# Optimization experiments

Measured on AMD Instinct MI355X. Metric: run time of the kernel, lower is better.

## Reference

```python
import jax, jax.numpy as jnp
import numpy as np

NUM_CLASSES = 1000
FEAT_DIM = 128
BATCH = 2048
ALPHA = 1.0


def setup_inputs() -> dict:
    key = jax.random.key(0)
    k1, k2, k3 = jax.random.split(key, 3)
    feat = jax.random.normal(k1, (BATCH, FEAT_DIM), dtype=jnp.float32)
    label = jax.random.randint(k2, (BATCH,), 0, NUM_CLASSES, dtype=jnp.int64)
    # centers ~ kaiming_uniform_(a=sqrt(5)) on a (C, D) matrix -> U(-b, b), b = sqrt(6/((1+5)*D)) = 1/sqrt(D)
    bound = 1.0 / np.sqrt(FEAT_DIM)
    centers = jax.random.uniform(k3, (NUM_CLASSES, FEAT_DIM), dtype=jnp.float32,
                                 minval=-bound, maxval=bound)
    return {"feat": feat, "label": label, "centers": centers}


def reference(feat, label, centers):
    # feat: [B, D], centers: [C, D], label: [B]
    batch_size = feat.shape[0]
    # squared euclidean distance to every center: [B, C]
    diff = feat[:, None, :] - centers[None, :, :]          # [B, C, D]
    dist = jnp.sum(diff * diff, axis=-1)                   # [B, C]
    # margin scaling: multiply true-class distance by (1 + alpha)
    y_onehot = jax.nn.one_hot(label, centers.shape[0], dtype=dist.dtype) * ALPHA + 1.0
    margin_dist = dist * y_onehot
    margin_logits = -0.5 * margin_dist
    logits = -0.5 * dist
    # likelihood regularizer: mean of half squared distance to own center
    cdiff = feat - centers[label]                          # [B, D]
    likelihood = (1.0 / batch_size) * jnp.sum(cdiff * cdiff) / 2.0
    return logits, margin_logits, likelihood
```

## Files before the change

kernel.cpp:

```cpp
#include <hip/hip_runtime.h>

#define BATCH 2048
#define NCLS  1000
#define FEAT  128

typedef short bf16x8 __attribute__((ext_vector_type(8)));
typedef float f32x16 __attribute__((ext_vector_type(16)));

__device__ __forceinline__ unsigned int f2bf(float f) {
    unsigned int u;
    __builtin_memcpy(&u, &f, 4);
    return (u + 0x7fffu + ((u >> 16) & 1u)) >> 16;
}

__device__ __forceinline__ bf16x8 cvt_chunk(const float* __restrict__ p, float& nrm) {
    float4 lo = *(const float4*)p;
    float4 hi = *(const float4*)(p + 4);
    nrm += lo.x * lo.x + lo.y * lo.y + lo.z * lo.z + lo.w * lo.w +
           hi.x * hi.x + hi.y * hi.y + hi.z * hi.z + hi.w * hi.w;
    bf16x8 r;
    r[0] = (short)f2bf(lo.x); r[1] = (short)f2bf(lo.y);
    r[2] = (short)f2bf(lo.z); r[3] = (short)f2bf(lo.w);
    r[4] = (short)f2bf(hi.x); r[5] = (short)f2bf(hi.y);
    r[6] = (short)f2bf(hi.z); r[7] = (short)f2bf(hi.w);
    return r;
}

__global__ __launch_bounds__(256) void lgm_fused(
    const float* __restrict__ feat,
    const float* __restrict__ centers,
    const int* __restrict__ label,
    float* __restrict__ ws,
    float* __restrict__ out)
{
    __shared__ float fn_lds[64];
    __shared__ float red[4];

    int tid     = threadIdx.x;
    int lane    = tid & 63;
    int wave    = tid >> 6;
    int tileCol = blockIdx.x & 15;
    int tileRow = blockIdx.x >> 4;
    int rowBase = tileRow * 64 + (wave & 1) * 32;
    int colBase = tileCol * 64 + (wave >> 1) * 32;
    int m       = lane & 31;
    int half    = lane >> 5;

    int r  = rowBase + m;
    int c0 = colBase + m;
    int c  = (c0 < NCLS) ? c0 : (NCLS - 1);

    const float* ap = feat    + r * FEAT + half * 8;
    const float* bp = centers + c * FEAT + half * 8;

    float fs = 0.0f, cs = 0.0f;
    f32x16 acc = {};
    #pragma unroll
    for (int kk = 0; kk < 8; kk++) {
        bf16x8 a = cvt_chunk(ap + kk * 16, fs);
        bf16x8 b = cvt_chunk(bp + kk * 16, cs);
        acc = __builtin_amdgcn_mfma_f32_32x32x16_bf16(a, b, acc, 0, 0, 0);
    }

    fs += __shfl_xor(fs, 32, 64);
    cs += __shfl_xor(cs, 32, 64);
    fn_lds[(wave & 1) * 32 + m] = fs;
    __syncthreads();

    float* out0 = out;
    float* out1 = out + BATCH * NCLS;
    float cnv   = cs;
    bool  colOK = (c0 < NCLS);
    int   rlb   = (wave & 1) * 32;
    float lsum  = 0.0f;
    #pragma unroll
    for (int reg = 0; reg < 16; reg++) {
        int rl  = rlb + (reg & 3) + 8 * (reg >> 2) + 4 * half;
        int row = tileRow * 64 + rl;
        if (colOK) {
            float dist  = fn_lds[rl] + cnv - 2.0f * acc[reg];
            float logit = -0.5f * dist;
            int   idx   = row * NCLS + c0;
            bool  match = (c0 == label[row]);
            out0[idx] = logit;
            out1[idx] = match ? 2.0f * logit : logit;
            if (match) lsum += dist;
        }
    }

    #pragma unroll
    for (int off = 32; off > 0; off >>= 1) lsum += __shfl_down(lsum, off, 64);
    if (lane == 0) red[wave] = lsum;
    __syncthreads();
    if (tid == 0) ws[blockIdx.x] = red[0] + red[1] + red[2] + red[3];
}

__global__ __launch_bounds__(64) void lgm_finish(
    const float* __restrict__ ws,
    float* __restrict__ out)
{
    int lane = threadIdx.x;
    float s = 0.0f;
    #pragma unroll
    for (int j = 0; j < 8; j++) s += ws[lane + 64 * j];
    #pragma unroll
    for (int off = 32; off > 0; off >>= 1) s += __shfl_down(s, off, 64);
    if (lane == 0) out[2 * BATCH * NCLS] = s * (0.5f / (float)BATCH);
}

extern "C" void kernel_launch(void* const* d_in, const int* in_sizes, int n_in,
                              void* d_out, int out_size, void* d_ws, size_t ws_size,
                              hipStream_t stream) {
    const float* feat    = (const float*)d_in[0];
    const int*   label   = (const int*)d_in[1];
    const float* centers = (const float*)d_in[2];
    float* ws = (float*)d_ws;

    lgm_fused<<<512, 256, 0, stream>>>(feat, centers, label, ws, (float*)d_out);
    lgm_finish<<<1, 64, 0, stream>>>(ws, (float*)d_out);
}
```

Baseline: 75.88 us.

## Stage bf16 tiles in swizzled LDS and compute likelihood directly per row

Each block now loads its 64-row feat tile and 64-row centers tile once with cooperative coalesced loads. It converts them to bf16 and writes them into XOR-swizzled shared memory, then feeds the MFMAs from LDS instead of having each wave reload and reconvert global data. Row and center norms are computed during staging. The likelihood term is now computed exactly in fp32 from feat minus the gathered center, only in tileCol 0 blocks, so the finish kernel reduces 32 partials instead of 512. The cost is about 33KB of LDS per block and an extra barrier, which may reduce occupancy. The kernel is dominated by output stores, so the gain is likely small.

Measured after the change: 71.65 us. 1.06x faster.

```diff
diff --git a/kernel.cpp b/kernel.cpp
--- a/kernel.cpp
+++ b/kernel.cpp
@@ -7,92 +7,149 @@
 typedef short bf16x8 __attribute__((ext_vector_type(8)));
 typedef float f32x16 __attribute__((ext_vector_type(16)));
 
-__device__ __forceinline__ unsigned int f2bf(float f) {
+#define WS_LP 0
+
+__device__ inline unsigned int f2bf(float f) {
     unsigned int u;
     __builtin_memcpy(&u, &f, 4);
     return (u + 0x7fffu + ((u >> 16) & 1u)) >> 16;
 }
 
-__device__ __forceinline__ bf16x8 cvt_chunk(const float* __restrict__ p, float& nrm) {
-    float4 lo = *(const float4*)p;
-    float4 hi = *(const float4*)(p + 4);
-    nrm += lo.x * lo.x + lo.y * lo.y + lo.z * lo.z + lo.w * lo.w +
-           hi.x * hi.x + hi.y * hi.y + hi.z * hi.z + hi.w * hi.w;
-    bf16x8 r;
-    r[0] = (short)f2bf(lo.x); r[1] = (short)f2bf(lo.y);
-    r[2] = (short)f2bf(lo.z); r[3] = (short)f2bf(lo.w);
-    r[4] = (short)f2bf(hi.x); r[5] = (short)f2bf(hi.y);
-    r[6] = (short)f2bf(hi.z); r[7] = (short)f2bf(hi.w);
-    return r;
-}
-
-__global__ __launch_bounds__(256) void lgm_fused(
+__global__ __launch_bounds__(256) void lgm_main_kernel(
     const float* __restrict__ feat,
     const float* __restrict__ centers,
     const int* __restrict__ label,
     float* __restrict__ ws,
     float* __restrict__ out)
 {
-    __shared__ float fn_lds[64];
-    __shared__ float red[4];
+    __shared__ __align__(16) unsigned char smem[33296];
+    unsigned char* sA  = smem;
+    unsigned char* sB  = smem + 16384;
+    float*         sFn = (float*)(smem + 32768);
+    float*         sCn = (float*)(smem + 33024);
+    float*         red = (float*)(smem + 33280);
 
     int tid     = threadIdx.x;
     int lane    = tid & 63;
     int wave    = tid >> 6;
     int tileCol = blockIdx.x & 15;
     int tileRow = blockIdx.x >> 4;
-    int rowBase = tileRow * 64 + (wave & 1) * 32;
-    int colBase = tileCol * 64 + (wave >> 1) * 32;
-    int m       = lane & 31;
-    int half    = lane >> 5;
+    int fr0     = tileRow * 64;
+    int cr0     = tileCol * 64;
 
-    int r  = rowBase + m;
-    int c0 = colBase + m;
-    int c  = (c0 < NCLS) ? c0 : (NCLS - 1);
+    int srow = tid >> 2;
+    int sq   = tid & 3;
 
-    const float* ap = feat    + r * FEAT + half * 8;
-    const float* bp = centers + c * FEAT + half * 8;
+    {
+        const float* src = feat + (fr0 + srow) * FEAT + sq * 32;
+        float v[32];
+        #pragma unroll
+        for (int j = 0; j < 8; j++) {
+            float4 t = ((const float4*)src)[j];
+            v[4*j+0] = t.x; v[4*j+1] = t.y; v[4*j+2] = t.z; v[4*j+3] = t.w;
+        }
+        float ns = 0.0f;
+        unsigned int w[16];
+        #pragma unroll
+        for (int i = 0; i < 16; i++) {
+            ns  += v[2*i] * v[2*i] + v[2*i+1] * v[2*i+1];
+            w[i] = f2bf(v[2*i]) | (f2bf(v[2*i+1]) << 16);
+        }
+        #pragma unroll
+        for (int s = 0; s < 4; s++) {
+            int off = sq * 64 + s * 16;
+            int swz = off ^ ((srow & 7) << 4);
+            uint4 t4; t4.x = w[4*s]; t4.y = w[4*s+1]; t4.z = w[4*s+2]; t4.w = w[4*s+3];
+            *(uint4*)(sA + srow * 256 + swz) = t4;
+        }
+        ns += __shfl_xor(ns, 1, 64);
+        ns += __shfl_xor(ns, 2, 64);
+        if (sq == 0) sFn[srow] = ns;
 
-    float fs = 0.0f, cs = 0.0f;
+        if (tileCol == 0) {
+            int lb = label[fr0 + srow];
+            const float* cl = centers + lb * FEAT + sq * 32;
+            float lsq = 0.0f;
+            #pragma unroll
+            for (int j = 0; j < 8; j++) {
+                float4 t = ((const float4*)cl)[j];
+                float d0 = v[4*j+0] - t.x, d1 = v[4*j+1] - t.y;
+                float d2 = v[4*j+2] - t.z, d3 = v[4*j+3] - t.w;
+                lsq += d0*d0 + d1*d1 + d2*d2 + d3*d3;
+            }
+            #pragma unroll
+            for (int off = 32; off > 0; off >>= 1) lsq += __shfl_down(lsq, off, 64);
+            if (lane == 0) red[wave] = lsq;
+        }
+    }
+
+    {
+        int cr  = cr0 + srow;
+        int crc = (cr < NCLS) ? cr : (NCLS - 1);
+        const float* src = centers + crc * FEAT + sq * 32;
+        float v[32];
+        #pragma unroll
+        for (int j = 0; j < 8; j++) {
+            float4 t = ((const float4*)src)[j];
+            v[4*j+0] = t.x; v[4*j+1] = t.y; v[4*j+2] = t.z; v[4*j+3] = t.w;
+        }
+        float ns = 0.0f;
+        unsigned int w[16];
+        #pragma unroll
+        for (int i = 0; i < 16; i++) {
+            ns  += v[2*i] * v[2*i] + v[2*i+1] * v[2*i+1];
+            w[i] = f2bf(v[2*i]) | (f2bf(v[2*i+1]) << 16);
+        }
+        #pragma unroll
+        for (int s = 0; s < 4; s++) {
+            int off = sq * 64 + s * 16;
+            int swz = off ^ ((srow & 7) << 4);
+            uint4 t4; t4.x = w[4*s]; t4.y = w[4*s+1]; t4.z = w[4*s+2]; t4.w = w[4*s+3];
+            *(uint4*)(sB + srow * 256 + swz) = t4;
+        }
+        ns += __shfl_xor(ns, 1, 64);
+        ns += __shfl_xor(ns, 2, 64);
+        if (sq == 0) sCn[srow] = ns;
+    }
+
+    __syncthreads();
+
+    if (tileCol == 0 && tid == 0)
+        ws[WS_LP + tileRow] = red[0] + red[1] + red[2] + red[3];
+
+    int m    = lane & 31;
+    int half = lane >> 5;
+    int rl   = (wave & 1) * 32 + m;
+    int cl_  = (wave >> 1) * 32 + m;
+    int rsw  = (rl  & 7) << 4;
+    int csw  = (cl_ & 7) << 4;
+
     f32x16 acc = {};
     #pragma unroll
     for (int kk = 0; kk < 8; kk++) {
-        bf16x8 a = cvt_chunk(ap + kk * 16, fs);
-        bf16x8 b = cvt_chunk(bp + kk * 16, cs);
+        int off = half * 16 + kk * 32;
+        bf16x8 a = *(const bf16x8*)(sA + rl  * 256 + (off ^ rsw));
+        bf16x8 b = *(const bf16x8*)(sB + cl_ * 256 + (off ^ csw));
         acc = __builtin_amdgcn_mfma_f32_32x32x16_bf16(a, b, acc, 0, 0, 0);
     }
 
-    fs += __shfl_xor(fs, 32, 64);
-    cs += __shfl_xor(cs, 32, 64);
-    fn_lds[(wave & 1) * 32 + m] = fs;
-    __syncthreads();
-
     float* out0 = out;
     float* out1 = out + BATCH * NCLS;
-    float cnv   = cs;
+    int   c0    = cr0 + (wave >> 1) * 32 + m;
+    float cnv   = sCn[(wave >> 1) * 32 + m];
     bool  colOK = (c0 < NCLS);
-    int   rlb   = (wave & 1) * 32;
-    float lsum  = 0.0f;
     #pragma unroll
     for (int reg = 0; reg < 16; reg++) {
-        int rl  = rlb + (reg & 3) + 8 * (reg >> 2) + 4 * half;
-        int row = tileRow * 64 + rl;
+        int rloc = (wave & 1) * 32 + (reg & 3) + 8 * (reg >> 2) + 4 * half;
+        int row  = fr0 + rloc;
         if (colOK) {
-            float dist  = fn_lds[rl] + cnv - 2.0f * acc[reg];
+            float dist  = sFn[rloc] + cnv - 2.0f * acc[reg];
             float logit = -0.5f * dist;
             int   idx   = row * NCLS + c0;
-            bool  match = (c0 == label[row]);
             out0[idx] = logit;
-            out1[idx] = match ? 2.0f * logit : logit;
-            if (match) lsum += dist;
+            out1[idx] = (c0 == label[row]) ? 2.0f * logit : logit;
         }
     }
-
-    #pragma unroll
-    for (int off = 32; off > 0; off >>= 1) lsum += __shfl_down(lsum, off, 64);
-    if (lane == 0) red[wave] = lsum;
-    __syncthreads();
-    if (tid == 0) ws[blockIdx.x] = red[0] + red[1] + red[2] + red[3];
 }
 
 __global__ __launch_bounds__(64) void lgm_finish(
@@ -100,9 +157,7 @@
     float* __restrict__ out)
 {
     int lane = threadIdx.x;
-    float s = 0.0f;
-    #pragma unroll
-    for (int j = 0; j < 8; j++) s += ws[lane + 64 * j];
+    float s = (lane < 32) ? ws[WS_LP + lane] : 0.0f;
     #pragma unroll
     for (int off = 32; off > 0; off >>= 1) s += __shfl_down(s, off, 64);
     if (lane == 0) out[2 * BATCH * NCLS] = s * (0.5f / (float)BATCH);
@@ -116,6 +171,6 @@
     const float* centers = (const float*)d_in[2];
     float* ws = (float*)d_ws;
 
-    lgm_fused<<<512, 256, 0, stream>>>(feat, centers, label, ws, (float*)d_out);
+    lgm_main_kernel<<<512, 256, 0, stream>>>(feat, centers, label, ws, (float*)d_out);
     lgm_finish<<<1, 64, 0, stream>>>(ws, (float*)d_out);
 }
```
